# Kernel optimization log

Measured on AMD Instinct MI355X. Metric: run time of the kernel, lower is better.

The kernel has to match this reference:

```python
import jax, jax.numpy as jnp
import numpy as np

B, N, C, H = 2, 2048, 768, 12
D = C // H  # head dim = 64


def _rotate_half(x):
    d2 = x.shape[-1] // 2
    x1, x2 = x[..., :d2], x[..., d2:]
    return jnp.concatenate([-x2, x1], axis=-1)


def _apply_rope(x, sin, cos):
    # x: [B,H,N,D], sin/cos: [N,D] -> broadcast over (B,H)
    return x * cos[None, None] + _rotate_half(x) * sin[None, None]


def setup_inputs() -> dict:
    key = jax.random.key(0)
    ks = jax.random.split(key, 7)
    x = jax.random.normal(ks[0], (B, N, C), dtype=jnp.float32)
    sin_spatial = jax.random.normal(ks[1], (N, D), dtype=jnp.float32)
    cos_spatial = jax.random.normal(ks[2], (N, D), dtype=jnp.float32)
    s = 1.0 / np.sqrt(C)
    W_qkv = jax.random.uniform(ks[3], (C, 3 * C), jnp.float32, -s, s)
    b_qkv = jax.random.uniform(ks[4], (3 * C,), jnp.float32, -s, s)
    W_out = jax.random.uniform(ks[5], (C, C), jnp.float32, -s, s)
    b_out = jax.random.uniform(ks[6], (C,), jnp.float32, -s, s)
    return {"x": x, "sin_spatial": sin_spatial, "cos_spatial": cos_spatial,
            "W_qkv": W_qkv, "b_qkv": b_qkv, "W_out": W_out, "b_out": b_out}


def reference(x, sin_spatial, cos_spatial, W_qkv, b_qkv, W_out, b_out):
    qkv = x @ W_qkv + b_qkv                       # [B,N,3C]
    qkv = qkv.reshape(B, N, 3, H, D).transpose(2, 0, 3, 1, 4)  # [3,B,H,N,D]
    q, k, v = qkv[0], qkv[1], qkv[2]
    q = _apply_rope(q, sin_spatial, cos_spatial)
    k = _apply_rope(k, sin_spatial, cos_spatial)
    att = jnp.einsum('bhqd,bhkd->bhqk', q, k) * (D ** -0.5)
    att = jax.nn.softmax(att, axis=-1)            # dropout is identity (eval)
    y = jnp.einsum('bhqk,bhkd->bhqd', att, v)     # [B,H,N,D]
    y = y.transpose(0, 2, 1, 3).reshape(B, N, C)
    return y @ W_out + b_out
```

## Files before the change

kernel.cpp:

```cpp
#include <hip/hip_runtime.h>
#include <hip/hip_bf16.h>

#define BB 2
#define NN 2048
#define CC 768
#define HH 12
#define DD 64
#define MM 4096
#define N3 2304

typedef __attribute__((ext_vector_type(8))) short bf16x8;
typedef __attribute__((ext_vector_type(4))) float f32x4;

#define QSCALE 0.18033688011112043f

__device__ __forceinline__ unsigned short f2bf(float f) {
    union { float f; unsigned u; } v; v.f = f;
    unsigned r = v.u + 0x7FFFu + ((v.u >> 16) & 1u);
    return (unsigned short)(r >> 16);
}

__device__ __forceinline__ float exp2_hw(float x) {
    float r;
    asm("v_exp_f32 %0, %1" : "=v"(r) : "v"(x));
    return r;
}

__device__ __forceinline__ bf16x8 ld_frag(const unsigned short* p) {
    bf16x8 r;
    __builtin_memcpy(&r, p, 8);
    __builtin_memcpy((char*)&r + 8, p + 16, 8);
    return r;
}

__global__ void k_cvt(const float* __restrict__ s, unsigned short* __restrict__ d, int n4) {
    int i = blockIdx.x * blockDim.x + threadIdx.x;
    int st = gridDim.x * blockDim.x;
    for (; i < n4; i += st) {
        float4 v = ((const float4*)s)[i];
        ushort4 o;
        o.x = f2bf(v.x); o.y = f2bf(v.y); o.z = f2bf(v.z); o.w = f2bf(v.w);
        ((ushort4*)d)[i] = o;
    }
}

__global__ void k_cvtT(const float* __restrict__ s, unsigned short* __restrict__ d,
                       int R, int Cc) {
    __shared__ unsigned short t[64][72];
    const int c0 = blockIdx.x * 64, r0 = blockIdx.y * 64;
    const int tr = threadIdx.x >> 4;
    const int tc = (threadIdx.x & 15) * 4;
#pragma unroll
    for (int i = 0; i < 4; i++) {
        int r = tr + i * 16;
        float4 v = *(const float4*)(s + (size_t)(r0 + r) * Cc + c0 + tc);
        t[tc + 0][r] = f2bf(v.x);
        t[tc + 1][r] = f2bf(v.y);
        t[tc + 2][r] = f2bf(v.z);
        t[tc + 3][r] = f2bf(v.w);
    }
    __syncthreads();
    const int wr = threadIdx.x >> 2;
    const int wc = (threadIdx.x & 3) * 16;
    *(uint4*)(d + (size_t)(c0 + wr) * R + r0 + wc)     = *(uint4*)&t[wr][wc];
    *(uint4*)(d + (size_t)(c0 + wr) * R + r0 + wc + 8) = *(uint4*)&t[wr][wc + 8];
}

__launch_bounds__(256)
__global__ void k_qkv(const unsigned short* __restrict__ xb,
                      const unsigned short* __restrict__ wt,
                      const float* __restrict__ bias,
                      const float* __restrict__ sinp,
                      const float* __restrict__ cosp,
                      unsigned short* __restrict__ qws,
                      unsigned short* __restrict__ kws,
                      unsigned short* __restrict__ vws) {
    __shared__ unsigned short As[128][40];
    __shared__ unsigned short Bs[64][40];
    const int tid = threadIdx.x;
    const int lane = tid & 63, w = tid >> 6;
    const int ql = lane & 15, lg = lane >> 4;
    const int row0 = blockIdx.x * 128;
    const int j0 = blockIdx.y * 64;

    f32x4 acc[2][4];
#pragma unroll
    for (int a = 0; a < 2; a++)
#pragma unroll
        for (int b = 0; b < 4; b++) acc[a][b] = f32x4{0.f, 0.f, 0.f, 0.f};

    const int ar = tid >> 1, ac = (tid & 1) * 16;
    const int jr = tid >> 2, kc = (tid & 3) * 8;

    for (int k0 = 0; k0 < CC; k0 += 32) {
        uint4 av0 = *(const uint4*)(xb + (size_t)(row0 + ar) * CC + k0 + ac);
        uint4 av1 = *(const uint4*)(xb + (size_t)(row0 + ar) * CC + k0 + ac + 8);
        uint4 bv  = *(const uint4*)(wt + (size_t)(j0 + jr) * CC + k0 + kc);
        *(uint4*)&As[ar][ac]     = av0;
        *(uint4*)&As[ar][ac + 8] = av1;
        *(uint4*)&Bs[jr][kc]     = bv;
        __syncthreads();

        bf16x8 af[2], bfr[4];
#pragma unroll
        for (int fr = 0; fr < 2; fr++) af[fr] = ld_frag(&As[w * 32 + fr * 16 + ql][lg * 4]);
#pragma unroll
        for (int fn = 0; fn < 4; fn++) bfr[fn] = ld_frag(&Bs[fn * 16 + ql][lg * 4]);
#pragma unroll
        for (int fr = 0; fr < 2; fr++)
#pragma unroll
            for (int fn = 0; fn < 4; fn++)
                acc[fr][fn] = __builtin_amdgcn_mfma_f32_16x16x32_bf16(af[fr], bfr[fn], acc[fr][fn], 0, 0, 0);
        __syncthreads();
    }

    float vals[2][4][4];
#pragma unroll
    for (int fr = 0; fr < 2; fr++)
#pragma unroll
        for (int fn = 0; fn < 4; fn++) {
            float bj = bias[j0 + fn * 16 + ql];
#pragma unroll
            for (int r = 0; r < 4; r++) vals[fr][fn][r] = acc[fr][fn][r] + bj;
        }
    const int t = j0 / CC;
    const int h = (j0 % CC) >> 6;
    if (t < 2) {
        unsigned short* outp = (t == 0) ? qws : kws;
        const float qs = (t == 0) ? QSCALE : 1.0f;
#pragma unroll
        for (int fr = 0; fr < 2; fr++)
#pragma unroll
            for (int r = 0; r < 4; r++) {
                int m = row0 + w * 32 + fr * 16 + lg * 4 + r;
                int b = m >> 11, n = m & (NN - 1);
#pragma unroll
                for (int fn = 0; fn < 4; fn++) {
                    int d = fn * 16 + ql;
                    float cv = cosp[n * DD + d], sv = sinp[n * DD + d];
                    float other = vals[fr][fn ^ 2][r];
                    float rv = (vals[fr][fn][r] * cv + ((fn < 2) ? -other : other) * sv) * qs;
                    outp[((size_t)(b * HH + h) * NN + n) * DD + d] = f2bf(rv);
                }
            }
    } else {
#pragma unroll
        for (int fr = 0; fr < 2; fr++)
#pragma unroll
            for (int r = 0; r < 4; r++) {
                int m = row0 + w * 32 + fr * 16 + lg * 4 + r;
                int b = m >> 11, n = m & (NN - 1);
#pragma unroll
                for (int fn = 0; fn < 4; fn++) {
                    int d = fn * 16 + ql;
                    vws[((size_t)(b * HH + h) * DD + d) * NN + n] = f2bf(vals[fr][fn][r]);
                }
            }
    }
}

__launch_bounds__(256)
__global__ void k_attn(const unsigned short* __restrict__ qws,
                       const unsigned short* __restrict__ kws,
                       const unsigned short* __restrict__ vws,
                       unsigned short* __restrict__ yws) {
    __shared__ unsigned short Ks[64][72];
    __shared__ unsigned short Vs[64][72];
    const int tid = threadIdx.x;
    const int lane = tid & 63, w = tid >> 6;
    const int ql = lane & 15, lg = lane >> 4;
    const int bh = blockIdx.y;
    const int qw = blockIdx.x * 64 + w * 16;
    const unsigned short* Qp = qws + (size_t)bh * NN * DD;
    const unsigned short* Kp = kws + (size_t)bh * NN * DD;
    const unsigned short* Vp = vws + (size_t)bh * DD * NN;

    bf16x8 qf[2];
#pragma unroll
    for (int kb = 0; kb < 2; kb++)
        qf[kb] = ld_frag(Qp + (size_t)(qw + ql) * DD + kb * 32 + lg * 4);

    f32x4 oacc[4];
#pragma unroll
    for (int a = 0; a < 4; a++) oacc[a] = f32x4{0.f, 0.f, 0.f, 0.f};
    float mrun = -1e30f, lrun = 0.f;

    const int sr = tid >> 2, sc = (tid & 3) * 16;

    for (int kt = 0; kt < NN / 64; kt++) {
        *(uint4*)&Ks[sr][sc]     = *(const uint4*)(Kp + (size_t)(kt * 64 + sr) * DD + sc);
        *(uint4*)&Ks[sr][sc + 8] = *(const uint4*)(Kp + (size_t)(kt * 64 + sr) * DD + sc + 8);
        *(uint4*)&Vs[sr][sc]     = *(const uint4*)(Vp + (size_t)sr * NN + kt * 64 + sc);
        *(uint4*)&Vs[sr][sc + 8] = *(const uint4*)(Vp + (size_t)sr * NN + kt * 64 + sc + 8);
        __syncthreads();

        f32x4 sacc[4];
#pragma unroll
        for (int a = 0; a < 4; a++) sacc[a] = f32x4{0.f, 0.f, 0.f, 0.f};
        __builtin_amdgcn_s_setprio(1);
#pragma unroll
        for (int kb = 0; kb < 2; kb++) {
            bf16x8 kf[4];
#pragma unroll
            for (int fr = 0; fr < 4; fr++) kf[fr] = ld_frag(&Ks[fr * 16 + ql][kb * 32 + lg * 4]);
#pragma unroll
            for (int fr = 0; fr < 4; fr++)
                sacc[fr] = __builtin_amdgcn_mfma_f32_16x16x32_bf16(kf[fr], qf[kb], sacc[fr], 0, 0, 0);
        }
        __builtin_amdgcn_s_setprio(0);

        float m0 = fmaxf(fmaxf(sacc[0][0], sacc[0][1]), fmaxf(sacc[0][2], sacc[0][3]));
        float m1 = fmaxf(fmaxf(sacc[1][0], sacc[1][1]), fmaxf(sacc[1][2], sacc[1][3]));
        float m2 = fmaxf(fmaxf(sacc[2][0], sacc[2][1]), fmaxf(sacc[2][2], sacc[2][3]));
        float m3 = fmaxf(fmaxf(sacc[3][0], sacc[3][1]), fmaxf(sacc[3][2], sacc[3][3]));
        float tm = fmaxf(fmaxf(m0, m1), fmaxf(m2, m3));
        tm = fmaxf(tm, __shfl_xor(tm, 16));
        tm = fmaxf(tm, __shfl_xor(tm, 32));
        if (__any(tm > mrun + 8.0f)) {
            float mn = fmaxf(mrun, tm);
            float scl = exp2_hw(mrun - mn);
            lrun *= scl;
#pragma unroll
            for (int db = 0; db < 4; db++) oacc[db] *= scl;
            mrun = mn;
        }
        float ts = 0.f;
#pragma unroll
        for (int fr = 0; fr < 4; fr++)
#pragma unroll
            for (int r = 0; r < 4; r++) {
                float p = exp2_hw(sacc[fr][r] - mrun);
                sacc[fr][r] = p;
                ts += p;
            }
        ts += __shfl_xor(ts, 16);
        ts += __shfl_xor(ts, 32);
        lrun += ts;

        bf16x8 pB[2];
#pragma unroll
        for (int kkb = 0; kkb < 2; kkb++) {
            bf16x8 t8;
#pragma unroll
            for (int e = 0; e < 8; e++)
                t8[e] = (short)f2bf(sacc[kkb * 2 + (e >> 2)][e & 3]);
            pB[kkb] = t8;
        }

        __builtin_amdgcn_s_setprio(1);
#pragma unroll
        for (int db = 0; db < 4; db++) {
            bf16x8 va[2];
#pragma unroll
            for (int kkb = 0; kkb < 2; kkb++) va[kkb] = ld_frag(&Vs[db * 16 + ql][kkb * 32 + lg * 4]);
#pragma unroll
            for (int kkb = 0; kkb < 2; kkb++)
                oacc[db] = __builtin_amdgcn_mfma_f32_16x16x32_bf16(va[kkb], pB[kkb], oacc[db], 0, 0, 0);
        }
        __builtin_amdgcn_s_setprio(0);
        __syncthreads();
    }

    const int b = bh / HH, h = bh % HH;
    float inv = 1.0f / lrun;
    int q = qw + ql;
#pragma unroll
    for (int db = 0; db < 4; db++)
#pragma unroll
        for (int r = 0; r < 4; r++) {
            int d = db * 16 + lg * 4 + r;
            yws[(size_t)(b * NN + q) * CC + h * DD + d] = f2bf(oacc[db][r] * inv);
        }
}

__launch_bounds__(256)
__global__ void k_out(const unsigned short* __restrict__ yb,
                      const unsigned short* __restrict__ wt,
                      const float* __restrict__ bias,
                      float* __restrict__ out) {
    __shared__ unsigned short As[128][40];
    __shared__ unsigned short Bs[64][40];
    const int tid = threadIdx.x;
    const int lane = tid & 63, w = tid >> 6;
    const int ql = lane & 15, lg = lane >> 4;
    const int row0 = blockIdx.x * 128;
    const int j0 = blockIdx.y * 64;

    f32x4 acc[2][4];
#pragma unroll
    for (int a = 0; a < 2; a++)
#pragma unroll
        for (int b = 0; b < 4; b++) acc[a][b] = f32x4{0.f, 0.f, 0.f, 0.f};

    const int ar = tid >> 1, ac = (tid & 1) * 16;
    const int jr = tid >> 2, kc = (tid & 3) * 8;

    for (int k0 = 0; k0 < CC; k0 += 32) {
        uint4 av0 = *(const uint4*)(yb + (size_t)(row0 + ar) * CC + k0 + ac);
        uint4 av1 = *(const uint4*)(yb + (size_t)(row0 + ar) * CC + k0 + ac + 8);
        uint4 bv  = *(const uint4*)(wt + (size_t)(j0 + jr) * CC + k0 + kc);
        *(uint4*)&As[ar][ac]     = av0;
        *(uint4*)&As[ar][ac + 8] = av1;
        *(uint4*)&Bs[jr][kc]     = bv;
        __syncthreads();

        bf16x8 af[2], bfr[4];
#pragma unroll
        for (int fr = 0; fr < 2; fr++) af[fr] = ld_frag(&As[w * 32 + fr * 16 + ql][lg * 4]);
#pragma unroll
        for (int fn = 0; fn < 4; fn++) bfr[fn] = ld_frag(&Bs[fn * 16 + ql][lg * 4]);
#pragma unroll
        for (int fr = 0; fr < 2; fr++)
#pragma unroll
            for (int fn = 0; fn < 4; fn++)
                acc[fr][fn] = __builtin_amdgcn_mfma_f32_16x16x32_bf16(af[fr], bfr[fn], acc[fr][fn], 0, 0, 0);
        __syncthreads();
    }

#pragma unroll
    for (int fr = 0; fr < 2; fr++)
#pragma unroll
        for (int fn = 0; fn < 4; fn++) {
            float bj = bias[j0 + fn * 16 + ql];
#pragma unroll
            for (int r = 0; r < 4; r++) {
                int m = row0 + w * 32 + fr * 16 + lg * 4 + r;
                out[(size_t)m * CC + j0 + fn * 16 + ql] = acc[fr][fn][r] + bj;
            }
        }
}

extern "C" void kernel_launch(void* const* d_in, const int* in_sizes, int n_in,
                              void* d_out, int out_size, void* d_ws, size_t ws_size,
                              hipStream_t stream) {
    const float* x    = (const float*)d_in[0];
    const float* sinp = (const float*)d_in[1];
    const float* cosp = (const float*)d_in[2];
    const float* wqkv = (const float*)d_in[3];
    const float* bqkv = (const float*)d_in[4];
    const float* wout = (const float*)d_in[5];
    const float* bout = (const float*)d_in[6];
    float* out = (float*)d_out;
    char* ws = (char*)d_ws;

    unsigned short* xb  = (unsigned short*)(ws);
    unsigned short* wqb = (unsigned short*)(ws + 6291456);
    unsigned short* wob = (unsigned short*)(ws + 9830400);
    unsigned short* qws = (unsigned short*)(ws + 11010048);
    unsigned short* kws = (unsigned short*)(ws + 17301504);
    unsigned short* vws = (unsigned short*)(ws + 23592960);
    unsigned short* yws = (unsigned short*)(ws + 29884416);
    if (ws_size < 36175872) return;

    k_cvt<<<dim3(512), dim3(256), 0, stream>>>(x, xb, MM * CC / 4);
    k_cvtT<<<dim3(36, 12), dim3(256), 0, stream>>>(wqkv, wqb, CC, N3);
    k_cvtT<<<dim3(12, 12), dim3(256), 0, stream>>>(wout, wob, CC, CC);
    k_qkv<<<dim3(32, 36), dim3(256), 0, stream>>>(xb, wqb, bqkv, sinp, cosp, qws, kws, vws);
    k_attn<<<dim3(32, 24), dim3(256), 0, stream>>>(qws, kws, vws, yws);
    k_out<<<dim3(32, 12), dim3(256), 0, stream>>>(yws, wob, bout, out);
}
```

Measured before the change: 142.4 us.

## Halve attention block size, remap grid for head locality, vectorize output stores

The attention kernel now runs 128-thread blocks that each cover 32 queries instead of 64, launched as a flat 1536-block grid. Consecutive block IDs are mapped across 8 heads so that neighbouring blocks share K/V tiles in cache. Each thread now loads twice as much K/V per tile, and the output is written as ushort4 vectors instead of scalar stores. The intent is more blocks in flight to fill the CUs and better L2 reuse, at the cost of more K/V reloads per query, since each block amortizes a tile over fewer queries.

```diff
diff --git a/kernel.cpp b/kernel.cpp
--- a/kernel.cpp
+++ b/kernel.cpp
@@ -159,7 +159,7 @@
     }
 }
 
-__launch_bounds__(256)
+__launch_bounds__(128)
 __global__ void k_attn(const unsigned short* __restrict__ qws,
                        const unsigned short* __restrict__ kws,
                        const unsigned short* __restrict__ vws,
@@ -169,8 +169,10 @@
     const int tid = threadIdx.x;
     const int lane = tid & 63, w = tid >> 6;
     const int ql = lane & 15, lg = lane >> 4;
-    const int bh = blockIdx.y;
-    const int qw = blockIdx.x * 64 + w * 16;
+    const int d0 = blockIdx.x;
+    const int bh = (d0 & 7) + 8 * (d0 >> 9);
+    const int qb = (d0 >> 3) & 63;
+    const int qw = qb * 32 + w * 16;
     const unsigned short* Qp = qws + (size_t)bh * NN * DD;
     const unsigned short* Kp = kws + (size_t)bh * NN * DD;
     const unsigned short* Vp = vws + (size_t)bh * DD * NN;
@@ -185,13 +187,17 @@
     for (int a = 0; a < 4; a++) oacc[a] = f32x4{0.f, 0.f, 0.f, 0.f};
     float mrun = -1e30f, lrun = 0.f;
 
-    const int sr = tid >> 2, sc = (tid & 3) * 16;
+    const int sr = tid >> 1, sh = (tid & 1) * 32;
 
     for (int kt = 0; kt < NN / 64; kt++) {
-        *(uint4*)&Ks[sr][sc]     = *(const uint4*)(Kp + (size_t)(kt * 64 + sr) * DD + sc);
-        *(uint4*)&Ks[sr][sc + 8] = *(const uint4*)(Kp + (size_t)(kt * 64 + sr) * DD + sc + 8);
-        *(uint4*)&Vs[sr][sc]     = *(const uint4*)(Vp + (size_t)sr * NN + kt * 64 + sc);
-        *(uint4*)&Vs[sr][sc + 8] = *(const uint4*)(Vp + (size_t)sr * NN + kt * 64 + sc + 8);
+        *(uint4*)&Ks[sr][sh]      = *(const uint4*)(Kp + (size_t)(kt * 64 + sr) * DD + sh);
+        *(uint4*)&Ks[sr][sh + 8]  = *(const uint4*)(Kp + (size_t)(kt * 64 + sr) * DD + sh + 8);
+        *(uint4*)&Ks[sr][sh + 16] = *(const uint4*)(Kp + (size_t)(kt * 64 + sr) * DD + sh + 16);
+        *(uint4*)&Ks[sr][sh + 24] = *(const uint4*)(Kp + (size_t)(kt * 64 + sr) * DD + sh + 24);
+        *(uint4*)&Vs[sr][sh]      = *(const uint4*)(Vp + (size_t)sr * NN + kt * 64 + sh);
+        *(uint4*)&Vs[sr][sh + 8]  = *(const uint4*)(Vp + (size_t)sr * NN + kt * 64 + sh + 8);
+        *(uint4*)&Vs[sr][sh + 16] = *(const uint4*)(Vp + (size_t)sr * NN + kt * 64 + sh + 16);
+        *(uint4*)&Vs[sr][sh + 24] = *(const uint4*)(Vp + (size_t)sr * NN + kt * 64 + sh + 24);
         __syncthreads();
 
         f32x4 sacc[4];
@@ -264,13 +270,16 @@
     const int b = bh / HH, h = bh % HH;
     float inv = 1.0f / lrun;
     int q = qw + ql;
-#pragma unroll
-    for (int db = 0; db < 4; db++)
-#pragma unroll
-        for (int r = 0; r < 4; r++) {
-            int d = db * 16 + lg * 4 + r;
-            yws[(size_t)(b * NN + q) * CC + h * DD + d] = f2bf(oacc[db][r] * inv);
-        }
+    unsigned short* yp = yws + (size_t)(b * NN + q) * CC + h * DD + lg * 4;
+#pragma unroll
+    for (int db = 0; db < 4; db++) {
+        ushort4 o;
+        o.x = f2bf(oacc[db][0] * inv);
+        o.y = f2bf(oacc[db][1] * inv);
+        o.z = f2bf(oacc[db][2] * inv);
+        o.w = f2bf(oacc[db][3] * inv);
+        *(ushort4*)(yp + db * 16) = o;
+    }
 }
 
 __launch_bounds__(256)
@@ -356,6 +365,6 @@
     k_cvtT<<<dim3(36, 12), dim3(256), 0, stream>>>(wqkv, wqb, CC, N3);
     k_cvtT<<<dim3(12, 12), dim3(256), 0, stream>>>(wout, wob, CC, CC);
     k_qkv<<<dim3(32, 36), dim3(256), 0, stream>>>(xb, wqb, bqkv, sinp, cosp, qws, kws, vws);
-    k_attn<<<dim3(32, 24), dim3(256), 0, stream>>>(qws, kws, vws, yws);
+    k_attn<<<dim3(1536), dim3(128), 0, stream>>>(qws, kws, vws, yws);
     k_out<<<dim3(32, 12), dim3(256), 0, stream>>>(yws, wob, bout, out);
 }
```

After: 149.8 us. 1.05x slower.
